# Performance work log

Hardware: AMD Instinct MI355X
Metric: run time of the kernel (lower is better)

The kernel has to match this reference:

```python
import jax, jax.numpy as jnp
import numpy as np

RADIUS, HEAD, SLOT, DIM = 16.0, 8, 112, 512

def _l2norm(x, axis):
    n = jnp.linalg.norm(x, axis=axis, keepdims=True)
    return x / jnp.maximum(n, 1e-12)

def _layernorm(x, g, b, eps=1e-5):
    mu = jnp.mean(x, axis=-1, keepdims=True)
    var = jnp.mean((x - mu) ** 2, axis=-1, keepdims=True)
    return (x - mu) / jnp.sqrt(var + eps) * g + b

def setup_inputs() -> dict:
    key = jax.random.key(0)
    ks = jax.random.split(key, 12)
    B, S = 32, 512
    return {
        "query": jax.random.normal(ks[0], (B, S, DIM), jnp.float32),
        "value": jax.random.normal(ks[1], (B, S, DIM), jnp.float32),
        "key_mem": jax.random.normal(ks[2], (HEAD * SLOT, DIM // HEAD), jnp.float32) * 0.5,
        "value_mem": jax.random.normal(ks[3], (SLOT, DIM), jnp.float32) * 0.5,
        "Wq": jax.random.normal(ks[4], (DIM, DIM), jnp.float32) * 0.02,
        "bq": jnp.zeros((DIM,), jnp.float32),
        "Wv": jax.random.normal(ks[5], (DIM, DIM), jnp.float32) * 0.02,
        "bv": jnp.zeros((DIM,), jnp.float32),
        "Wl": jax.random.normal(ks[6], (DIM, DIM * HEAD), jnp.float32) * 0.02,
        "bl": jnp.zeros((DIM,), jnp.float32),
        "g1": jnp.ones((DIM,), jnp.float32), "b1": jnp.zeros((DIM,), jnp.float32),
        "g2": jnp.ones((DIM,), jnp.float32), "b2": jnp.zeros((DIM,), jnp.float32),
        "g3": jnp.ones((DIM,), jnp.float32), "b3": jnp.zeros((DIM,), jnp.float32),
    }

def reference(query, value, key_mem, value_mem, Wq, bq, Wv, bv, Wl, bl,
              g1, b1, g2, b2, g3, b3):
    B, S, C = query.shape
    mq = query.reshape(B * S, C)                                   # (BS, 512)
    # --- key addressing (read path) ---
    key_norm = _l2norm(key_mem.reshape(HEAD, SLOT, -1), axis=2)    # (h, s, 64)
    eq = _l2norm((mq @ Wq.T + bq).reshape(B * S, HEAD, -1), axis=2)
    key_sim = jnp.einsum('bhd,hsd->bhs', eq, key_norm)             # (BS, h, s)
    key_add = jax.nn.softmax(RADIUS * key_sim, axis=2)
    m_head = jnp.einsum('bhs,sd->bhd', key_add,
                        jax.lax.stop_gradient(value_mem))          # (BS, h, 512)
    vir = _layernorm(m_head.reshape(B * S, HEAD * DIM) @ Wl.T + bl, g2, b2)
    te_fusion = _layernorm(query + vir.reshape(B, S, DIM), g1, b1)  # dropout = eval identity
    # --- value addressing (write/train path) ---
    mv = value.reshape(B * S, DIM)
    ev = jax.lax.stop_gradient(mv) @ Wv.T + bv
    value_norm = _l2norm(value_mem, axis=1)                        # (s, 512)
    value_sim = _l2norm(ev, axis=1) @ value_norm.T                 # (BS, s)
    value_add = jax.nn.softmax(RADIUS * value_sim, axis=1)
    aud = value_add @ value_mem                                    # (BS, 512)
    contrastive = 0.5 * jnp.abs(jnp.eye(SLOT, dtype=value_norm.dtype)
                                - value_norm @ value_norm.T).sum()[None]
    mvd = jax.lax.stop_gradient(mv)
    cos = (aud * mvd).sum(1) / jnp.maximum(
        jnp.linalg.norm(aud, axis=1) * jnp.linalg.norm(mvd, axis=1), 1e-8)
    recon = jnp.abs(1.0 - cos).reshape(B, S).sum(1)                # (B,)
    aud = _layernorm(aud, g3, b3)
    tr_fusion = _layernorm(query + aud.reshape(B, S, DIM), g1, b1)
    return (te_fusion, tr_fusion, recon, contrastive)
```

## Files before the change

kernel.cpp:

```cpp
#include <hip/hip_runtime.h>
#include <math.h>

#define DIMC   512
#define HEADS  8
#define SLOTS  112
#define HD     64
#define NROWS  16384
#define RADIUSF 16.0f

typedef short short8 __attribute__((ext_vector_type(8)));
typedef unsigned short ushort8 __attribute__((ext_vector_type(8)));
typedef float f32x4  __attribute__((ext_vector_type(4)));

__device__ __forceinline__ unsigned short f2bf(float f)
{
    unsigned u = __float_as_uint(f);
    unsigned r = (u + 0x7FFFu + ((u >> 16) & 1u)) >> 16;
    return (unsigned short)r;
}
__device__ __forceinline__ float bf2f(unsigned short h)
{
    return __uint_as_float((unsigned)h << 16);
}

__device__ __forceinline__ void gl16(const void* g, void* lds_wave_base)
{
    __builtin_amdgcn_global_load_lds(
        (const __attribute__((address_space(1))) unsigned int*)g,
        (__attribute__((address_space(3))) unsigned int*)lds_wave_base,
        16, 0, 0);
}

#define DPP_ADD(x, ctrl, rmask)                                               \
    (x) += __int_as_float(__builtin_amdgcn_update_dpp(                        \
               0, __float_as_int(x), (ctrl), (rmask), 0xf, true))

__device__ __forceinline__ float wsum64(float x)
{
    DPP_ADD(x, 0x111, 0xf);
    DPP_ADD(x, 0x112, 0xf);
    DPP_ADD(x, 0x114, 0xf);
    DPP_ADD(x, 0x118, 0xf);
    DPP_ADD(x, 0x142, 0xa);
    DPP_ADD(x, 0x143, 0xc);
    return __int_as_float(__builtin_amdgcn_readlane(__float_as_int(x), 63));
}

__device__ __forceinline__ void wsum64_4(float& a, float& b, float& c, float& d)
{
    DPP_ADD(a, 0x111, 0xf); DPP_ADD(b, 0x111, 0xf); DPP_ADD(c, 0x111, 0xf); DPP_ADD(d, 0x111, 0xf);
    DPP_ADD(a, 0x112, 0xf); DPP_ADD(b, 0x112, 0xf); DPP_ADD(c, 0x112, 0xf); DPP_ADD(d, 0x112, 0xf);
    DPP_ADD(a, 0x114, 0xf); DPP_ADD(b, 0x114, 0xf); DPP_ADD(c, 0x114, 0xf); DPP_ADD(d, 0x114, 0xf);
    DPP_ADD(a, 0x118, 0xf); DPP_ADD(b, 0x118, 0xf); DPP_ADD(c, 0x118, 0xf); DPP_ADD(d, 0x118, 0xf);
    DPP_ADD(a, 0x142, 0xa); DPP_ADD(b, 0x142, 0xa); DPP_ADD(c, 0x142, 0xa); DPP_ADD(d, 0x142, 0xa);
    DPP_ADD(a, 0x143, 0xc); DPP_ADD(b, 0x143, 0xc); DPP_ADD(c, 0x143, 0xc); DPP_ADD(d, 0x143, 0xc);
    a = __int_as_float(__builtin_amdgcn_readlane(__float_as_int(a), 63));
    b = __int_as_float(__builtin_amdgcn_readlane(__float_as_int(b), 63));
    c = __int_as_float(__builtin_amdgcn_readlane(__float_as_int(c), 63));
    d = __int_as_float(__builtin_amdgcn_readlane(__float_as_int(d), 63));
}

__global__ __launch_bounds__(256)
void gemm_bf16(const short* __restrict__ A, int lda,
               const short* __restrict__ B, int ldb,
               float* __restrict__ C, unsigned short* __restrict__ Cb,
               int ldc, int K, const float* __restrict__ bias, int Nvalid,
               int aZ, int bZ, int cZ)
{
    __shared__ short As[128 * 32];
    __shared__ short Bs[128 * 32];
    A += (size_t)blockIdx.z * aZ;
    B += (size_t)blockIdx.z * bZ;
    const size_t czoff = (size_t)blockIdx.z * cZ;
    const int tid  = threadIdx.x;
    const int wave = tid >> 6;
    const int lane = tid & 63;
    const int m0 = blockIdx.y * 128;
    const int n0 = blockIdx.x * 128;
    const int wm = (wave >> 1) * 64;
    const int wn = (wave & 1) * 64;

    const int srow = tid >> 2;
    const int schk = (tid & 3) * 8;

    const int fr = lane & 15;
    const int fq = (lane >> 4) * 8;

    f32x4 acc[4][4] = {};

    const short* Ag = A + (size_t)(m0 + srow) * lda + schk;
    const short* Bg = B + (size_t)(n0 + srow) * ldb + schk;

    short* asL = As + wave * 512;
    short* asU = As + 2048 + wave * 512;
    short* bsL = Bs + wave * 512;
    short* bsU = Bs + 2048 + wave * 512;

    for (int k0 = 0; k0 < K; k0 += 32) {
        gl16(Ag, asL);
        gl16(Ag + (size_t)64 * lda, asU);
        gl16(Bg, bsL);
        gl16(Bg + (size_t)64 * ldb, bsU);
        Ag += 32; Bg += 32;
        __syncthreads();
        short8 af[4], bf[4];
        #pragma unroll
        for (int i = 0; i < 4; ++i)
            af[i] = *(const short8*)&As[(wm + i * 16 + fr) * 32 + fq];
        #pragma unroll
        for (int j = 0; j < 4; ++j)
            bf[j] = *(const short8*)&Bs[(wn + j * 16 + fr) * 32 + fq];
        #pragma unroll
        for (int i = 0; i < 4; ++i)
            #pragma unroll
            for (int j = 0; j < 4; ++j)
                acc[i][j] = __builtin_amdgcn_mfma_f32_16x16x32_bf16(
                    af[i], bf[j], acc[i][j], 0, 0, 0);
        __syncthreads();
    }

    const int cr = (lane >> 4) * 4;
    const int cc = lane & 15;
    #pragma unroll
    for (int i = 0; i < 4; ++i) {
        const int grow = m0 + wm + i * 16 + cr;
        #pragma unroll
        for (int j = 0; j < 4; ++j) {
            const int gcol = n0 + wn + j * 16 + cc;
            if (gcol < Nvalid) {
                const float bb = bias ? bias[gcol] : 0.f;
                const size_t base = czoff + (size_t)grow * ldc + gcol;
                #pragma unroll
                for (int r = 0; r < 4; ++r) {
                    const float val = acc[i][j][r] + bb;
                    if (C)  C[base + (size_t)r * ldc]  = val;
                    if (Cb) Cb[base + (size_t)r * ldc] = f2bf(val);
                }
            }
        }
    }
}

__global__ __launch_bounds__(256)
void gemm_softmax(const short* __restrict__ A, int lda, int aZ,
                  const short* __restrict__ B, int ldb, int bZ,
                  int K,
                  const float* __restrict__ sc, int scStride,
                  unsigned short* __restrict__ Ob, int ldo, int oPerZ, int padN)
{
    __shared__ short As[128 * 32];
    __shared__ short Bs[128 * 32];
    __shared__ float P[128][113];
    A += (size_t)blockIdx.z * aZ;
    B += (size_t)blockIdx.z * bZ;
    const int tid  = threadIdx.x;
    const int wave = tid >> 6;
    const int lane = tid & 63;
    const int m0 = blockIdx.y * 128;
    const int wm = (wave >> 1) * 64;
    const int wn = (wave & 1) * 64;
    const int srow = tid >> 2;
    const int schk = (tid & 3) * 8;
    const int fr = lane & 15;
    const int fq = (lane >> 4) * 8;

    f32x4 acc[4][4] = {};

    const short* Ag = A + (size_t)(m0 + srow) * lda + schk;
    const short* Bg = B + (size_t)srow * ldb + schk;

    short* asL = As + wave * 512;
    short* asU = As + 2048 + wave * 512;
    short* bsL = Bs + wave * 512;
    short* bsU = Bs + 2048 + wave * 512;

    for (int k0 = 0; k0 < K; k0 += 32) {
        gl16(Ag, asL);
        gl16(Ag + (size_t)64 * lda, asU);
        gl16(Bg, bsL);
        gl16(Bg + (size_t)64 * ldb, bsU);
        Ag += 32; Bg += 32;
        __syncthreads();
        short8 af[4], bf[4];
        #pragma unroll
        for (int i = 0; i < 4; ++i)
            af[i] = *(const short8*)&As[(wm + i * 16 + fr) * 32 + fq];
        #pragma unroll
        for (int j = 0; j < 4; ++j)
            bf[j] = *(const short8*)&Bs[(wn + j * 16 + fr) * 32 + fq];
        #pragma unroll
        for (int i = 0; i < 4; ++i)
            #pragma unroll
            for (int j = 0; j < 4; ++j)
                acc[i][j] = __builtin_amdgcn_mfma_f32_16x16x32_bf16(
                    af[i], bf[j], acc[i][j], 0, 0, 0);
        __syncthreads();
    }

    const int cr = (lane >> 4) * 4;
    const int cc = lane & 15;
    #pragma unroll
    for (int i = 0; i < 4; ++i) {
        const int prow = wm + i * 16 + cr;
        #pragma unroll
        for (int j = 0; j < 4; ++j) {
            const int pcol = wn + j * 16 + cc;
            if (pcol < SLOTS) {
                #pragma unroll
                for (int r = 0; r < 4; ++r)
                    P[prow + r][pcol] = acc[i][j][r];
            }
        }
    }
    __syncthreads();

    const int rowt = tid >> 1;
    const int half = tid & 1;
    const int k0 = half * 56;
    const int rr = m0 + rowt;
    const float s = RADIUSF * sc[(size_t)rr * scStride + blockIdx.z];
    float mx = -1e30f;
    for (int k = k0; k < k0 + 56; ++k) mx = fmaxf(mx, P[rowt][k]);
    mx = fmaxf(mx, __shfl_xor(mx, 1, 64));
    float sum = 0.f;
    for (int k = k0; k < k0 + 56; ++k) {
        const float e = __expf(s * (P[rowt][k] - mx));
        P[rowt][k] = e;
        sum += e;
    }
    sum += __shfl_xor(sum, 1, 64);
    const float inv = 1.f / sum;
    unsigned short* orow = Ob + (size_t)rr * ldo + (size_t)blockIdx.z * oPerZ;
    for (int k = k0; k < k0 + 56; ++k) orow[k] = f2bf(P[rowt][k] * inv);
    if (half == 1)
        for (int k = SLOTS; k < padN; ++k) orow[k] = 0;
}

__device__ __forceinline__ float block_sum_256(float v, float* red)
{
    #pragma unroll
    for (int off = 32; off; off >>= 1) v += __shfl_down(v, off, 64);
    const int lane = threadIdx.x & 63, wid = threadIdx.x >> 6;
    __syncthreads();
    if (lane == 0) red[wid] = v;
    __syncthreads();
    return red[0] + red[1] + red[2] + red[3];
}

__global__ void zero_small(float* p, int n)
{
    int i = blockIdx.x * blockDim.x + threadIdx.x;
    if (i < n) p[i] = 0.f;
}

__global__ void f32_to_bf16(const float* __restrict__ src,
                            unsigned short* __restrict__ dst, int n)
{
    int i = (blockIdx.x * blockDim.x + threadIdx.x) * 4;
    if (i >= n) return;
    float4 v = *(const float4*)(src + i);
    ushort4 o;
    o.x = f2bf(v.x); o.y = f2bf(v.y); o.z = f2bf(v.z); o.w = f2bf(v.w);
    *(ushort4*)(dst + i) = o;
}

__global__ void prep_key_norm(const float* __restrict__ km,
                              unsigned short* __restrict__ knb)
{
    const int row = blockIdx.x;
    const int h = row >> 7, s = row & 127;
    const int lane = threadIdx.x;
    const float v = (s < SLOTS) ? km[(size_t)(h * SLOTS + s) * HD + lane] : 0.f;
    const float ssum = wsum64(v * v);
    const float inv = 1.f / fmaxf(sqrtf(ssum), 1e-12f);
    knb[(size_t)row * HD + lane] = f2bf(v * inv);
}

__global__ void prep_value_norm(const float* __restrict__ vm,
                                float* __restrict__ vn,
                                unsigned short* __restrict__ vnb,
                                unsigned short* __restrict__ vmTb)
{
    const int row = blockIdx.x;
    const int tid = threadIdx.x;
    __shared__ float red[4];
    const float v0 = vm[(size_t)row * DIMC + tid];
    const float v1 = vm[(size_t)row * DIMC + 256 + tid];
    const float tot = block_sum_256(v0 * v0 + v1 * v1, red);
    const float inv = 1.f / fmaxf(sqrtf(tot), 1e-12f);
    vn[(size_t)row * DIMC + tid]        = v0 * inv;
    vn[(size_t)row * DIMC + 256 + tid]  = v1 * inv;
    vnb[(size_t)row * DIMC + tid]       = f2bf(v0 * inv);
    vnb[(size_t)row * DIMC + 256 + tid] = f2bf(v1 * inv);
    vmTb[(size_t)tid * 128 + row]         = f2bf(v0);
    vmTb[(size_t)(256 + tid) * 128 + row] = f2bf(v1);
}

__global__ void contrastive_kernel(const float* __restrict__ vn, float* __restrict__ outc)
{
    __shared__ float vni[DIMC];
    __shared__ float red[2];
    const int i = blockIdx.x, tid = threadIdx.x;
    for (int d = tid; d < DIMC; d += 128) vni[d] = vn[(size_t)i * DIMC + d];
    __syncthreads();
    float t = 0.f;
    if (tid < SLOTS) {
        const float* r = vn + (size_t)tid * DIMC;
        float dot = 0.f;
        for (int d = 0; d < DIMC; ++d) dot += vni[d] * r[d];
        const float delta = (tid == i) ? 1.f : 0.f;
        t = fabsf(delta - dot);
    }
    #pragma unroll
    for (int off = 32; off; off >>= 1) t += __shfl_down(t, off, 64);
    if ((tid & 63) == 0) red[tid >> 6] = t;
    __syncthreads();
    if (tid == 0) atomicAdd(outc, 0.5f * (red[0] + red[1]));
}

__global__ __launch_bounds__(256)
void eq_head_norms(const unsigned short* __restrict__ eq, float* __restrict__ hinv)
{
    const int wid  = threadIdx.x >> 6;
    const int lane = threadIdx.x & 63;
    const int r = blockIdx.x * 4 + wid;
    const ushort8 u = *(const ushort8*)(eq + (size_t)r * DIMC + lane * 8);
    float s = 0.f;
    #pragma unroll
    for (int i = 0; i < 8; ++i) {
        const float f = bf2f(u[i]);
        s += f * f;
    }
    DPP_ADD(s, 0x111, 0xf);
    DPP_ADD(s, 0x112, 0xf);
    DPP_ADD(s, 0x114, 0xf);
    if ((lane & 7) == 7)
        hinv[(size_t)r * HEADS + (lane >> 3)] = 1.f / fmaxf(sqrtf(s), 1e-12f);
}

__global__ __launch_bounds__(256)
void row_rnorm(const unsigned short* __restrict__ x, float* __restrict__ rinv)
{
    const int wave = threadIdx.x >> 6, lane = threadIdx.x & 63;
    const int r = blockIdx.x * 4 + wave;
    const ushort8 u = *(const ushort8*)(x + (size_t)r * DIMC + lane * 8);
    float s = 0.f;
    #pragma unroll
    for (int i = 0; i < 8; ++i) {
        const float f = bf2f(u[i]);
        s += f * f;
    }
    s = wsum64(s);
    if (lane == 0) rinv[r] = 1.f / fmaxf(sqrtf(s), 1e-12f);
}

__global__ __launch_bounds__(256, 4)
void vir_te_w(const float* __restrict__ vir_pre, const float* __restrict__ query,
              const float* __restrict__ g1, const float* __restrict__ b1,
              const float* __restrict__ g2, const float* __restrict__ b2,
              float* __restrict__ out_te)
{
    const int wave = threadIdx.x >> 6, lane = threadIdx.x & 63;
    const int r0 = blockIdx.x * 8 + wave * 2;
    const int c0 = lane * 8;

    float x[2][8], q[2][8];
    #pragma unroll
    for (int p = 0; p < 2; ++p) {
        const size_t base = (size_t)(r0 + p) * DIMC + c0;
        *(f32x4*)&x[p][0] = *(const f32x4*)(vir_pre + base);
        *(f32x4*)&x[p][4] = *(const f32x4*)(vir_pre + base + 4);
        *(f32x4*)&q[p][0] = *(const f32x4*)(query + base);
        *(f32x4*)&q[p][4] = *(const f32x4*)(query + base + 4);
    }
    float gg2[8], bb2[8], gg1[8], bb1[8];
    *(f32x4*)&gg2[0] = *(const f32x4*)(g2 + c0);
    *(f32x4*)&gg2[4] = *(const f32x4*)(g2 + c0 + 4);
    *(f32x4*)&bb2[0] = *(const f32x4*)(b2 + c0);
    *(f32x4*)&bb2[4] = *(const f32x4*)(b2 + c0 + 4);
    *(f32x4*)&gg1[0] = *(const f32x4*)(g1 + c0);
    *(f32x4*)&gg1[4] = *(const f32x4*)(g1 + c0 + 4);
    *(f32x4*)&bb1[0] = *(const f32x4*)(b1 + c0);
    *(f32x4*)&bb1[4] = *(const f32x4*)(b1 + c0 + 4);

    float s1[2] = {0.f, 0.f}, s2[2] = {0.f, 0.f};
    #pragma unroll
    for (int p = 0; p < 2; ++p)
        #pragma unroll
        for (int i = 0; i < 8; ++i) {
            s1[p] += x[p][i];
            s2[p] += x[p][i] * x[p][i];
        }
    wsum64_4(s1[0], s2[0], s1[1], s2[1]);

    float y[2][8];
    float t1[2] = {0.f, 0.f}, t2[2] = {0.f, 0.f};
    #pragma unroll
    for (int p = 0; p < 2; ++p) {
        const float mu = s1[p] * (1.f / DIMC);
        const float var = s2[p] * (1.f / DIMC) - mu * mu;
        const float rstd = rsqrtf(var + 1e-5f);
        #pragma unroll
        for (int i = 0; i < 8; ++i) {
            const float v = (x[p][i] - mu) * rstd * gg2[i] + bb2[i];
            y[p][i] = q[p][i] + v;
            t1[p] += y[p][i];
            t2[p] += y[p][i] * y[p][i];
        }
    }
    wsum64_4(t1[0], t2[0], t1[1], t2[1]);

    #pragma unroll
    for (int p = 0; p < 2; ++p) {
        const float mu = t1[p] * (1.f / DIMC);
        const float var = t2[p] * (1.f / DIMC) - mu * mu;
        const float rstd = rsqrtf(var + 1e-5f);
        float o[8];
        #pragma unroll
        for (int i = 0; i < 8; ++i)
            o[i] = (y[p][i] - mu) * rstd * gg1[i] + bb1[i];
        const size_t base = (size_t)(r0 + p) * DIMC + c0;
        *(float4*)(out_te + base)     = make_float4(o[0], o[1], o[2], o[3]);
        *(float4*)(out_te + base + 4) = make_float4(o[4], o[5], o[6], o[7]);
    }
}

__global__ __launch_bounds__(256, 4)
void aud_epilogue_w(const float* __restrict__ aud, const float* __restrict__ value,
                    const float* __restrict__ query,
                    const float* __restrict__ g1, const float* __restrict__ b1,
                    const float* __restrict__ g3, const float* __restrict__ b3,
                    float* __restrict__ out_tr, float* __restrict__ recon)
{
    __shared__ float red[4];
    const int wave = threadIdx.x >> 6, lane = threadIdx.x & 63;
    const int r0 = blockIdx.x * 8 + wave * 2;
    const int c0 = lane * 8;

    float a[2][8], v[2][8], q[2][8];
    #pragma unroll
    for (int p = 0; p < 2; ++p) {
        const size_t base = (size_t)(r0 + p) * DIMC + c0;
        *(f32x4*)&a[p][0] = *(const f32x4*)(aud + base);
        *(f32x4*)&a[p][4] = *(const f32x4*)(aud + base + 4);
        *(f32x4*)&v[p][0] = *(const f32x4*)(value + base);
        *(f32x4*)&v[p][4] = *(const f32x4*)(value + base + 4);
        *(f32x4*)&q[p][0] = *(const f32x4*)(query + base);
        *(f32x4*)&q[p][4] = *(const f32x4*)(query + base + 4);
    }
    float gg3[8], bb3[8], gg1[8], bb1[8];
    *(f32x4*)&gg3[0] = *(const f32x4*)(g3 + c0);
    *(f32x4*)&gg3[4] = *(const f32x4*)(g3 + c0 + 4);
    *(f32x4*)&bb3[0] = *(const f32x4*)(b3 + c0);
    *(f32x4*)&bb3[4] = *(const f32x4*)(b3 + c0 + 4);
    *(f32x4*)&gg1[0] = *(const f32x4*)(g1 + c0);
    *(f32x4*)&gg1[4] = *(const f32x4*)(g1 + c0 + 4);
    *(f32x4*)&bb1[0] = *(const f32x4*)(b1 + c0);
    *(f32x4*)&bb1[4] = *(const f32x4*)(b1 + c0 + 4);

    float dot[2] = {0.f, 0.f}, na[2] = {0.f, 0.f};
    float nv[2] = {0.f, 0.f}, s1[2] = {0.f, 0.f};
    #pragma unroll
    for (int p = 0; p < 2; ++p)
        #pragma unroll
        for (int i = 0; i < 8; ++i) {
            dot[p] += a[p][i] * v[p][i];
            na[p]  += a[p][i] * a[p][i];
            nv[p]  += v[p][i] * v[p][i];
            s1[p]  += a[p][i];
        }
    wsum64_4(dot[0], na[0], nv[0], s1[0]);
    wsum64_4(dot[1], na[1], nv[1], s1[1]);

    float rloc = 0.f;
    #pragma unroll
    for (int p = 0; p < 2; ++p) {
        const float cosv = dot[p] / fmaxf(sqrtf(na[p]) * sqrtf(nv[p]), 1e-8f);
        rloc += fabsf(1.f - cosv);
    }
    if (lane == 0) red[wave] = rloc;

    float y[2][8];
    float t1[2] = {0.f, 0.f}, t2[2] = {0.f, 0.f};
    #pragma unroll
    for (int p = 0; p < 2; ++p) {
        const float mu = s1[p] * (1.f / DIMC);
        const float var = na[p] * (1.f / DIMC) - mu * mu;
        const float rstd = rsqrtf(var + 1e-5f);
        #pragma unroll
        for (int i = 0; i < 8; ++i) {
            const float w = (a[p][i] - mu) * rstd * gg3[i] + bb3[i];
            y[p][i] = q[p][i] + w;
            t1[p] += y[p][i];
            t2[p] += y[p][i] * y[p][i];
        }
    }
    wsum64_4(t1[0], t2[0], t1[1], t2[1]);

    #pragma unroll
    for (int p = 0; p < 2; ++p) {
        const float mu = t1[p] * (1.f / DIMC);
        const float var = t2[p] * (1.f / DIMC) - mu * mu;
        const float rstd = rsqrtf(var + 1e-5f);
        float o[8];
        #pragma unroll
        for (int i = 0; i < 8; ++i)
            o[i] = (y[p][i] - mu) * rstd * gg1[i] + bb1[i];
        const size_t base = (size_t)(r0 + p) * DIMC + c0;
        *(float4*)(out_tr + base)     = make_float4(o[0], o[1], o[2], o[3]);
        *(float4*)(out_tr + base + 4) = make_float4(o[4], o[5], o[6], o[7]);
    }

    __syncthreads();
    if (threadIdx.x == 0)
        atomicAdd(&recon[r0 >> 9], red[0] + red[1] + red[2] + red[3]);
}

extern "C" void kernel_launch(void* const* d_in, const int* in_sizes, int n_in,
                              void* d_out, int out_size, void* d_ws, size_t ws_size,
                              hipStream_t stream)
{
    const float* query = (const float*)d_in[0];
    const float* value = (const float*)d_in[1];
    const float* keym  = (const float*)d_in[2];
    const float* vmem  = (const float*)d_in[3];
    const float* Wq    = (const float*)d_in[4];
    const float* bq    = (const float*)d_in[5];
    const float* Wv    = (const float*)d_in[6];
    const float* bv    = (const float*)d_in[7];
    const float* Wl    = (const float*)d_in[8];
    const float* bl    = (const float*)d_in[9];
    const float* g1    = (const float*)d_in[10];
    const float* b1    = (const float*)d_in[11];
    const float* g2    = (const float*)d_in[12];
    const float* b2    = (const float*)d_in[13];
    const float* g3    = (const float*)d_in[14];
    const float* b3    = (const float*)d_in[15];

    float* out    = (float*)d_out;
    float* out_te = out;
    float* out_tr = out + 8388608;
    float* out_rc = out + 16777216;

    float* ws = (float*)d_ws;
    unsigned short* w_knb  = (unsigned short*)(ws + 0);
    unsigned short* w_vmTb = (unsigned short*)(ws + 32768);
    unsigned short* w_vnb  = (unsigned short*)(ws + 65536);
    float*          w_vn   = ws + 98304;
    unsigned short* w_w2tbf= (unsigned short*)(ws + 155648);
    float*          w_hinv = ws + 385024;
    unsigned short* w_vmbf = (unsigned short*)(ws + 516096);
    unsigned short* w_wlbf = (unsigned short*)(ws + 548864);
    float*          w_big1 = ws + 1597440;
    unsigned short* w_xbf  = (unsigned short*)(ws + 9986048);
    unsigned short* w_kaddc= (unsigned short*)(ws + 14180352);
    unsigned short* w_vsb  = (unsigned short*)(ws + 21520384);
    unsigned short* w_qbf  = (unsigned short*)(ws + 22568960);
    unsigned short* w_wqbf = (unsigned short*)(ws + 26763264);
    float*          w_rinv = ws + 26894336;

    zero_small<<<1, 64, 0, stream>>>(out_rc, 33);
    zero_small<<<256, 256, 0, stream>>>(ws + 32768, 65536);
    zero_small<<<128, 256, 0, stream>>>(ws + 516096, 32768);

    prep_key_norm<<<1024, 64, 0, stream>>>(keym, w_knb);
    prep_value_norm<<<112, 256, 0, stream>>>(vmem, w_vn, w_vnb, w_vmTb);
    contrastive_kernel<<<112, 128, 0, stream>>>(w_vn, out_rc + 32);
    f32_to_bf16<<<2048, 256, 0, stream>>>(Wl, w_wlbf, DIMC * DIMC * HEADS);
    f32_to_bf16<<<56, 256, 0, stream>>>(vmem, w_vmbf, SLOTS * DIMC);
    gemm_bf16<<<dim3(1, 4, 8), 256, 0, stream>>>(
        (const short*)w_wlbf, HEADS * DIMC, (const short*)w_vmbf, DIMC,
        nullptr, w_w2tbf, HEADS * SLOTS, DIMC, nullptr, SLOTS,
        DIMC, 0, SLOTS);

    f32_to_bf16<<<8192, 256, 0, stream>>>(query, w_qbf, NROWS * DIMC);
    f32_to_bf16<<<256, 256, 0, stream>>>(Wq, w_wqbf, DIMC * DIMC);
    gemm_bf16<<<dim3(4, 128), 256, 0, stream>>>(
        (const short*)w_qbf, DIMC, (const short*)w_wqbf, DIMC,
        nullptr, w_xbf, DIMC, DIMC, bq, DIMC, 0, 0, 0);
    eq_head_norms<<<NROWS / 4, 256, 0, stream>>>(w_xbf, w_hinv);
    gemm_softmax<<<dim3(1, 128, 8), 256, 0, stream>>>(
        (const short*)w_xbf, DIMC, HD, (const short*)w_knb, HD, 128 * HD,
        HD, w_hinv, HEADS, w_kaddc, HEADS * SLOTS, SLOTS, SLOTS);
    gemm_bf16<<<dim3(4, 128), 256, 0, stream>>>(
        (const short*)w_kaddc, HEADS * SLOTS, (const short*)w_w2tbf, HEADS * SLOTS,
        w_big1, nullptr, DIMC, HEADS * SLOTS, bl, DIMC, 0, 0, 0);
    vir_te_w<<<NROWS / 8, 256, 0, stream>>>(w_big1, query, g1, b1, g2, b2, out_te);

    f32_to_bf16<<<8192, 256, 0, stream>>>(value, w_qbf, NROWS * DIMC);
    f32_to_bf16<<<256, 256, 0, stream>>>(Wv, w_wqbf, DIMC * DIMC);
    gemm_bf16<<<dim3(4, 128), 256, 0, stream>>>(
        (const short*)w_qbf, DIMC, (const short*)w_wqbf, DIMC,
        nullptr, w_xbf, DIMC, DIMC, bv, DIMC, 0, 0, 0);
    row_rnorm<<<NROWS / 4, 256, 0, stream>>>(w_xbf, w_rinv);
    gemm_softmax<<<dim3(1, 128, 1), 256, 0, stream>>>(
        (const short*)w_xbf, DIMC, 0, (const short*)w_vnb, DIMC, 0,
        DIMC, w_rinv, 1, w_vsb, 128, 0, 128);
    gemm_bf16<<<dim3(4, 128), 256, 0, stream>>>(
        (const short*)w_vsb, 128, (const short*)w_vmTb, 128,
        w_big1, nullptr, DIMC, 128, nullptr, DIMC, 0, 0, 0);
    aud_epilogue_w<<<NROWS / 8, 256, 0, stream>>>(
        w_big1, value, query, g1, b1, g3, b3, out_tr, out_rc);
}
```

Baseline: 388.2 us.

## Fuse row norms into gemm_softmax and merge conversions/zeroing into fewer launches

Computes the per-row (or per-head) L2 norm of the A operand inside gemm_softmax from the bf16 fragments already loaded for the MFMA, removing the separate eq_head_norms and row_rnorm kernels and their extra read of the projected activations. All fp32-to-bf16 conversions (query, value, Wq, Wv, Wl, value_mem) are merged into one conv_all launch, and the zero-fill kernels are folded into prep_key_norm and prep_value_norm. This cuts launch count and memory passes, at the cost of extra VALU work in the GEMM inner loop and a larger workspace, since value and Wv now get their own buffers.

```diff
diff --git a/kernel.cpp b/kernel.cpp
--- a/kernel.cpp
+++ b/kernel.cpp
@@ -145,12 +145,12 @@
 void gemm_softmax(const short* __restrict__ A, int lda, int aZ,
                   const short* __restrict__ B, int ldb, int bZ,
                   int K,
-                  const float* __restrict__ sc, int scStride,
                   unsigned short* __restrict__ Ob, int ldo, int oPerZ, int padN)
 {
     __shared__ short As[128 * 32];
     __shared__ short Bs[128 * 32];
     __shared__ float P[128][113];
+    __shared__ float hinvS[128];
     A += (size_t)blockIdx.z * aZ;
     B += (size_t)blockIdx.z * bZ;
     const int tid  = threadIdx.x;
@@ -165,6 +165,7 @@
     const int fq = (lane >> 4) * 8;
 
     f32x4 acc[4][4] = {};
+    float ss[4] = {0.f, 0.f, 0.f, 0.f};
 
     const short* Ag = A + (size_t)(m0 + srow) * lda + schk;
     const short* Bg = B + (size_t)srow * ldb + schk;
@@ -191,10 +192,28 @@
         #pragma unroll
         for (int i = 0; i < 4; ++i)
             #pragma unroll
+            for (int e = 0; e < 8; ++e) {
+                const float f = bf2f((unsigned short)af[i][e]);
+                ss[i] += f * f;
+            }
+        #pragma unroll
+        for (int i = 0; i < 4; ++i)
+            #pragma unroll
             for (int j = 0; j < 4; ++j)
                 acc[i][j] = __builtin_amdgcn_mfma_f32_16x16x32_bf16(
                     af[i], bf[j], acc[i][j], 0, 0, 0);
         __syncthreads();
+    }
+
+    #pragma unroll
+    for (int i = 0; i < 4; ++i) {
+        ss[i] += __shfl_xor(ss[i], 16, 64);
+        ss[i] += __shfl_xor(ss[i], 32, 64);
+    }
+    if (lane < 16) {
+        #pragma unroll
+        for (int i = 0; i < 4; ++i)
+            hinvS[wm + i * 16 + lane] = 1.f / fmaxf(sqrtf(ss[i]), 1e-12f);
     }
 
     const int cr = (lane >> 4) * 4;
@@ -218,7 +237,7 @@
     const int half = tid & 1;
     const int k0 = half * 56;
     const int rr = m0 + rowt;
-    const float s = RADIUSF * sc[(size_t)rr * scStride + blockIdx.z];
+    const float s = RADIUSF * hinvS[rowt];
     float mx = -1e30f;
     for (int k = k0; k < k0 + 56; ++k) mx = fmaxf(mx, P[rowt][k]);
     mx = fmaxf(mx, __shfl_xor(mx, 1, 64));
@@ -247,29 +266,42 @@
     return red[0] + red[1] + red[2] + red[3];
 }
 
-__global__ void zero_small(float* p, int n)
-{
-    int i = blockIdx.x * blockDim.x + threadIdx.x;
-    if (i < n) p[i] = 0.f;
-}
-
-__global__ void f32_to_bf16(const float* __restrict__ src,
-                            unsigned short* __restrict__ dst, int n)
-{
-    int i = (blockIdx.x * blockDim.x + threadIdx.x) * 4;
-    if (i >= n) return;
-    float4 v = *(const float4*)(src + i);
+__global__ void conv_all(const float* __restrict__ q, const float* __restrict__ v,
+                         const float* __restrict__ Wq, const float* __restrict__ Wv,
+                         const float* __restrict__ Wl, const float* __restrict__ vm,
+                         unsigned short* __restrict__ qbf, unsigned short* __restrict__ vbf,
+                         unsigned short* __restrict__ wqbf, unsigned short* __restrict__ wvbf,
+                         unsigned short* __restrict__ wlbf, unsigned short* __restrict__ vmbf)
+{
+    const int i = blockIdx.x * blockDim.x + threadIdx.x;
+    const float* src;
+    unsigned short* dst;
+    int off;
+    if (i < 2097152)      { src = q;  dst = qbf;  off = i; }
+    else if (i < 4194304) { src = v;  dst = vbf;  off = i - 2097152; }
+    else if (i < 4259840) { src = Wq; dst = wqbf; off = i - 4194304; }
+    else if (i < 4325376) { src = Wv; dst = wvbf; off = i - 4259840; }
+    else if (i < 4849664) { src = Wl; dst = wlbf; off = i - 4325376; }
+    else if (i < 4864000) { src = vm; dst = vmbf; off = i - 4849664; }
+    else {
+        const int j = i - 4864000;
+        *(ushort4*)(vmbf + 57344 + (size_t)j * 4) = make_ushort4(0, 0, 0, 0);
+        return;
+    }
+    const float4 x = *(const float4*)(src + (size_t)off * 4);
     ushort4 o;
-    o.x = f2bf(v.x); o.y = f2bf(v.y); o.z = f2bf(v.z); o.w = f2bf(v.w);
-    *(ushort4*)(dst + i) = o;
+    o.x = f2bf(x.x); o.y = f2bf(x.y); o.z = f2bf(x.z); o.w = f2bf(x.w);
+    *(ushort4*)(dst + (size_t)off * 4) = o;
 }
 
 __global__ void prep_key_norm(const float* __restrict__ km,
-                              unsigned short* __restrict__ knb)
+                              unsigned short* __restrict__ knb,
+                              float* __restrict__ outrc)
 {
     const int row = blockIdx.x;
     const int h = row >> 7, s = row & 127;
     const int lane = threadIdx.x;
+    if (row == 0 && lane < 33) outrc[lane] = 0.f;
     const float v = (s < SLOTS) ? km[(size_t)(h * SLOTS + s) * HD + lane] : 0.f;
     const float ssum = wsum64(v * v);
     const float inv = 1.f / fmaxf(sqrtf(ssum), 1e-12f);
@@ -283,6 +315,16 @@
 {
     const int row = blockIdx.x;
     const int tid = threadIdx.x;
+    if (row >= 112) {
+        const int idx = (row - 112) * 256 + tid;
+        if (idx < 8192) {
+            vmTb[(size_t)(idx >> 4) * 128 + 112 + (idx & 15)] = 0;
+        } else {
+            const int j = idx - 8192;
+            vnb[(size_t)(112 + (j >> 9)) * 512 + (j & 511)] = 0;
+        }
+        return;
+    }
     __shared__ float red[4];
     const float v0 = vm[(size_t)row * DIMC + tid];
     const float v1 = vm[(size_t)row * DIMC + 256 + tid];
@@ -316,42 +358,6 @@
     if ((tid & 63) == 0) red[tid >> 6] = t;
     __syncthreads();
     if (tid == 0) atomicAdd(outc, 0.5f * (red[0] + red[1]));
-}
-
-__global__ __launch_bounds__(256)
-void eq_head_norms(const unsigned short* __restrict__ eq, float* __restrict__ hinv)
-{
-    const int wid  = threadIdx.x >> 6;
-    const int lane = threadIdx.x & 63;
-    const int r = blockIdx.x * 4 + wid;
-    const ushort8 u = *(const ushort8*)(eq + (size_t)r * DIMC + lane * 8);
-    float s = 0.f;
-    #pragma unroll
-    for (int i = 0; i < 8; ++i) {
-        const float f = bf2f(u[i]);
-        s += f * f;
-    }
-    DPP_ADD(s, 0x111, 0xf);
-    DPP_ADD(s, 0x112, 0xf);
-    DPP_ADD(s, 0x114, 0xf);
-    if ((lane & 7) == 7)
-        hinv[(size_t)r * HEADS + (lane >> 3)] = 1.f / fmaxf(sqrtf(s), 1e-12f);
-}
-
-__global__ __launch_bounds__(256)
-void row_rnorm(const unsigned short* __restrict__ x, float* __restrict__ rinv)
-{
-    const int wave = threadIdx.x >> 6, lane = threadIdx.x & 63;
-    const int r = blockIdx.x * 4 + wave;
-    const ushort8 u = *(const ushort8*)(x + (size_t)r * DIMC + lane * 8);
-    float s = 0.f;
-    #pragma unroll
-    for (int i = 0; i < 8; ++i) {
-        const float f = bf2f(u[i]);
-        s += f * f;
-    }
-    s = wsum64(s);
-    if (lane == 0) rinv[r] = 1.f / fmaxf(sqrtf(s), 1e-12f);
 }
 
 __global__ __launch_bounds__(256, 4)
@@ -548,7 +554,6 @@
     unsigned short* w_vnb  = (unsigned short*)(ws + 65536);
     float*          w_vn   = ws + 98304;
     unsigned short* w_w2tbf= (unsigned short*)(ws + 155648);
-    float*          w_hinv = ws + 385024;
     unsigned short* w_vmbf = (unsigned short*)(ws + 516096);
     unsigned short* w_wlbf = (unsigned short*)(ws + 548864);
     float*          w_big1 = ws + 1597440;
@@ -556,46 +561,38 @@
     unsigned short* w_kaddc= (unsigned short*)(ws + 14180352);
     unsigned short* w_vsb  = (unsigned short*)(ws + 21520384);
     unsigned short* w_qbf  = (unsigned short*)(ws + 22568960);
-    unsigned short* w_wqbf = (unsigned short*)(ws + 26763264);
-    float*          w_rinv = ws + 26894336;
-
-    zero_small<<<1, 64, 0, stream>>>(out_rc, 33);
-    zero_small<<<256, 256, 0, stream>>>(ws + 32768, 65536);
-    zero_small<<<128, 256, 0, stream>>>(ws + 516096, 32768);
-
-    prep_key_norm<<<1024, 64, 0, stream>>>(keym, w_knb);
-    prep_value_norm<<<112, 256, 0, stream>>>(vmem, w_vn, w_vnb, w_vmTb);
+    unsigned short* w_vbf  = (unsigned short*)(ws + 26763264);
+    unsigned short* w_wqbf = (unsigned short*)(ws + 30957568);
+    unsigned short* w_wvbf = (unsigned short*)(ws + 31088640);
+
+    conv_all<<<19008, 256, 0, stream>>>(query, value, Wq, Wv, Wl, vmem,
+                                        w_qbf, w_vbf, w_wqbf, w_wvbf,
+                                        w_wlbf, w_vmbf);
+    prep_key_norm<<<1024, 64, 0, stream>>>(keym, w_knb, out_rc);
+    prep_value_norm<<<176, 256, 0, stream>>>(vmem, w_vn, w_vnb, w_vmTb);
     contrastive_kernel<<<112, 128, 0, stream>>>(w_vn, out_rc + 32);
-    f32_to_bf16<<<2048, 256, 0, stream>>>(Wl, w_wlbf, DIMC * DIMC * HEADS);
-    f32_to_bf16<<<56, 256, 0, stream>>>(vmem, w_vmbf, SLOTS * DIMC);
     gemm_bf16<<<dim3(1, 4, 8), 256, 0, stream>>>(
         (const short*)w_wlbf, HEADS * DIMC, (const short*)w_vmbf, DIMC,
         nullptr, w_w2tbf, HEADS * SLOTS, DIMC, nullptr, SLOTS,
         DIMC, 0, SLOTS);
 
-    f32_to_bf16<<<8192, 256, 0, stream>>>(query, w_qbf, NROWS * DIMC);
-    f32_to_bf16<<<256, 256, 0, stream>>>(Wq, w_wqbf, DIMC * DIMC);
     gemm_bf16<<<dim3(4, 128), 256, 0, stream>>>(
         (const short*)w_qbf, DIMC, (const short*)w_wqbf, DIMC,
         nullptr, w_xbf, DIMC, DIMC, bq, DIMC, 0, 0, 0);
-    eq_head_norms<<<NROWS / 4, 256, 0, stream>>>(w_xbf, w_hinv);
     gemm_softmax<<<dim3(1, 128, 8), 256, 0, stream>>>(
         (const short*)w_xbf, DIMC, HD, (const short*)w_knb, HD, 128 * HD,
-        HD, w_hinv, HEADS, w_kaddc, HEADS * SLOTS, SLOTS, SLOTS);
+        HD, w_kaddc, HEADS * SLOTS, SLOTS, SLOTS);
     gemm_bf16<<<dim3(4, 128), 256, 0, stream>>>(
         (const short*)w_kaddc, HEADS * SLOTS, (const short*)w_w2tbf, HEADS * SLOTS,
         w_big1, nullptr, DIMC, HEADS * SLOTS, bl, DIMC, 0, 0, 0);
     vir_te_w<<<NROWS / 8, 256, 0, stream>>>(w_big1, query, g1, b1, g2, b2, out_te);
 
-    f32_to_bf16<<<8192, 256, 0, stream>>>(value, w_qbf, NROWS * DIMC);
-    f32_to_bf16<<<256, 256, 0, stream>>>(Wv, w_wqbf, DIMC * DIMC);
     gemm_bf16<<<dim3(4, 128), 256, 0, stream>>>(
-        (const short*)w_qbf, DIMC, (const short*)w_wqbf, DIMC,
+        (const short*)w_vbf, DIMC, (const short*)w_wvbf, DIMC,
         nullptr, w_xbf, DIMC, DIMC, bv, DIMC, 0, 0, 0);
-    row_rnorm<<<NROWS / 4, 256, 0, stream>>>(w_xbf, w_rinv);
     gemm_softmax<<<dim3(1, 128, 1), 256, 0, stream>>>(
         (const short*)w_xbf, DIMC, 0, (const short*)w_vnb, DIMC, 0,
-        DIMC, w_rinv, 1, w_vsb, 128, 0, 128);
+        DIMC, w_vsb, 128, 0, 128);
     gemm_bf16<<<dim3(4, 128), 256, 0, stream>>>(
         (const short*)w_vsb, 128, (const short*)w_vmTb, 128,
         w_big1, nullptr, DIMC, 128, nullptr, DIMC, 0, 0, 0);
```

Measured after the change: 359.8 us. -7.3%, faster.
